# Performance work log

Hardware: AMD Instinct MI355X
Metric: run time of the kernel (lower is better)

The kernel has to match this reference:

```python
import jax, jax.numpy as jnp
import numpy as np

# Degree-sorted atom layout (DeepChem convention): atoms of degree d are contiguous.
D_COUNTS = [8192, 65536, 131072, 196608, 98304, 16384, 8192]  # degrees 0..6
OFFSETS = np.cumsum([0] + D_COUNTS)  # start index of each degree block
N_ATOMS = int(OFFSETS[-1])           # 524288
F_IN = 75
BATCH = 16384
MAX_DEG = 6
BN_EPS = 1e-3


def setup_inputs() -> dict:
    key = jax.random.key(0)
    ks = jax.random.split(key, 40)
    inp = {}
    inp["atom_features"] = jax.random.normal(ks[0], (N_ATOMS, F_IN), jnp.float32)
    # every molecule gets exactly N_ATOMS/BATCH atoms -> all segments populated
    inp["membership"] = (jnp.arange(N_ATOMS, dtype=jnp.int32) % BATCH)
    for d in range(1, MAX_DEG + 1):
        inp[f"adj{d}"] = jax.random.randint(ks[d], (D_COUNTS[d], d), 0, N_ATOMS, dtype=jnp.int32)
    # GraphConv weights: 2*MAX_DEG + 1 = 13 matrices (rel/self per degree 1..6, self for degree 0)
    inp["gc1_W"] = jax.random.normal(ks[10], (13, F_IN, 32), jnp.float32) * 0.1
    inp["gc1_b"] = jax.random.normal(ks[11], (13, 32), jnp.float32) * 0.01
    inp["gc2_W"] = jax.random.normal(ks[12], (13, 32, 32), jnp.float32) * 0.1
    inp["gc2_b"] = jax.random.normal(ks[13], (13, 32), jnp.float32) * 0.01
    inp["bn1_gamma"] = jnp.ones((32,), jnp.float32)
    inp["bn1_beta"] = jnp.zeros((32,), jnp.float32)
    inp["bn1_mean"] = jax.random.normal(ks[14], (32,), jnp.float32) * 0.1
    inp["bn1_var"] = jax.random.uniform(ks[15], (32,), jnp.float32, 0.5, 1.5)
    inp["bn3_gamma"] = jnp.ones((64,), jnp.float32)
    inp["bn3_beta"] = jnp.zeros((64,), jnp.float32)
    inp["bn3_mean"] = jax.random.normal(ks[16], (64,), jnp.float32) * 0.1
    inp["bn3_var"] = jax.random.uniform(ks[17], (64,), jnp.float32, 0.5, 1.5)
    inp["d1_W"] = jax.random.normal(ks[18], (32, 64), jnp.float32) * 0.1
    inp["d1_b"] = jnp.zeros((64,), jnp.float32)
    inp["d2_W"] = jax.random.normal(ks[19], (128, 1), jnp.float32) * 0.1
    inp["d2_b"] = jnp.zeros((1,), jnp.float32)
    inp["d3_W"] = jnp.array([0.5, -1, -1, 1, 1, 1, 1, 1, -1, -1, -1, -1, -1, -1, -1, -1], jnp.float32)[:, None]
    inp["d3_b"] = jnp.zeros((1,), jnp.float32)
    inp["x_add"] = jax.random.normal(ks[20], (BATCH, 15), jnp.float32)
    inp["batch_size"] = BATCH
    return inp


def _batch_norm(x, gamma, beta, mean, var):
    return gamma * (x - mean) * jax.lax.rsqrt(var + BN_EPS) + beta


def _graph_conv(atoms, adjs, W, b):
    # atoms: [N, F]; adjs[d-1]: [n_d, d] neighbor indices for degree-d atoms
    outs = []
    for d in range(1, MAX_DEG + 1):
        s, n = int(OFFSETS[d]), D_COUNTS[d]
        rel = atoms[adjs[d - 1]].sum(axis=1)          # [n_d, F] summed neighbors
        self_a = atoms[s:s + n]                        # [n_d, F]
        wr, br = W[2 * (d - 1)], b[2 * (d - 1)]
        ws, bs = W[2 * (d - 1) + 1], b[2 * (d - 1) + 1]
        outs.append(rel @ wr + br + self_a @ ws + bs)
    out0 = atoms[:D_COUNTS[0]] @ W[12] + b[12]         # degree-0: self only
    return jnp.tanh(jnp.concatenate([out0] + outs, axis=0))


def _graph_pool(atoms, adjs):
    outs = [atoms[:D_COUNTS[0]]]  # degree-0 passthrough
    for d in range(1, MAX_DEG + 1):
        s, n = int(OFFSETS[d]), D_COUNTS[d]
        self_a = atoms[s:s + n]
        neigh_max = atoms[adjs[d - 1]].max(axis=1)     # [n_d, F]
        outs.append(jnp.maximum(self_a, neigh_max))    # max over {self} U neighbors
    return jnp.concatenate(outs, axis=0)


def reference(atom_features, membership, adj1, adj2, adj3, adj4, adj5, adj6,
              gc1_W, gc1_b, gc2_W, gc2_b,
              bn1_gamma, bn1_beta, bn1_mean, bn1_var,
              bn3_gamma, bn3_beta, bn3_mean, bn3_var,
              d1_W, d1_b, d2_W, d2_b, d3_W, d3_b, x_add, batch_size):
    adjs = [adj1, adj2, adj3, adj4, adj5, adj6]
    h = _graph_conv(atom_features, adjs, gc1_W, gc1_b)          # [N, 32], tanh
    h = _batch_norm(h, bn1_gamma, bn1_beta, bn1_mean, bn1_var)
    h = _graph_pool(h, adjs)
    h = _graph_conv(h, adjs, gc2_W, gc2_b)                      # [N, 32]
    # NOTE: original reuses batch_norm1 here (source does self.batch_norm1 twice)
    h = _batch_norm(h, bn1_gamma, bn1_beta, bn1_mean, bn1_var)
    h = _graph_pool(h, adjs)
    h = jnp.tanh(h @ d1_W + d1_b)                               # [N, 64]
    h = _batch_norm(h, bn3_gamma, bn3_beta, bn3_mean, bn3_var)
    # GraphGather: per-molecule sum and max readout
    sum_r = jax.ops.segment_sum(h, membership, num_segments=batch_size)
    max_r = jax.ops.segment_max(h, membership, num_segments=batch_size)
    mol = jnp.tanh(jnp.concatenate([sum_r, max_r], axis=1))     # [B, 128]
    model_var = mol @ d2_W + d2_b                               # [B, 1]
    binding = jnp.concatenate([model_var, x_add], axis=1)       # [B, 16]
    ans = binding @ d3_W + d3_b                                 # [B, 1]
    return ans.reshape(1, -1)
```

## Files before the change

### kernel.cpp

```cpp
#include <hip/hip_runtime.h>

typedef unsigned short u16;
typedef __bf16 bf8v __attribute__((ext_vector_type(8)));
typedef float f32x4 __attribute__((ext_vector_type(4)));

#define N_ATOMS 524288
#define NROW32  16777216

#define P_EP1   0
#define P_EP2   224
#define P_BN1   448
#define P_BN3   576
#define P_D1WT  832
#define P_D1B   2880
#define P_D2W   2944
#define P_SC    3072

__device__ __forceinline__ float b2f(u16 u) {
  return __builtin_bit_cast(float, ((unsigned)u) << 16);
}
__device__ __forceinline__ u16 f2b(float f) {
  unsigned x = __builtin_bit_cast(unsigned, f);
  x += 0x7fffu + ((x >> 16) & 1u);
  return (u16)(x >> 16);
}
__device__ __forceinline__ float ldf(const void* p, size_t i, int isbf) {
  return isbf ? b2f(((const u16*)p)[i]) : ((const float*)p)[i];
}
__device__ __forceinline__ u16 ldb(const void* p, size_t i, int isbf) {
  return isbf ? ((const u16*)p)[i] : f2b(((const float*)p)[i]);
}

__device__ __forceinline__ float exp2_fast(float x) {
#if __has_builtin(__builtin_amdgcn_exp2f)
  return __builtin_amdgcn_exp2f(x);
#else
  return exp2f(x);
#endif
}
__device__ __forceinline__ float rcp_fast(float x) {
#if __has_builtin(__builtin_amdgcn_rcpf)
  return __builtin_amdgcn_rcpf(x);
#else
  return 1.0f / x;
#endif
}
__device__ __forceinline__ float tanh_fast(float x) {
  float xc = fminf(fmaxf(x, -15.f), 15.f);
  float t = exp2_fast(xc * -2.8853900817779268f);
  return (1.f - t) * rcp_fast(1.f + t);
}

__device__ __forceinline__ void seg_of(int r, int& d, int& off) {
  if      (r < 8192)   { d = 0; off = 0; }
  else if (r < 73728)  { d = 1; off = 8192; }
  else if (r < 204800) { d = 2; off = 73728; }
  else if (r < 401408) { d = 3; off = 204800; }
  else if (r < 499712) { d = 4; off = 401408; }
  else if (r < 516096) { d = 5; off = 499712; }
  else                 { d = 6; off = 516096; }
}

__global__ void probe_kernel(const void* __restrict__ atoms, int* __restrict__ flag) {
  int lane = threadIdx.x;
  unsigned u = ((const u16*)atoms)[(size_t)lane * 148];
  int e = (u >> 7) & 0xFF;
  bool ok = (e >= 100 && e <= 140);
  unsigned long long b = __ballot(ok);
  if (lane == 0) flag[0] = (__popcll(b) >= 48) ? 1 : 0;
}

__global__ __launch_bounds__(64) void prep_kernel(
    const void* gW1, const void* gB1, const void* gW2, const void* gB2,
    const void* b1g, const void* b1b, const void* b1m, const void* b1v,
    const void* g3, const void* b3, const void* m3, const void* v3,
    const void* d1W, const void* d1b, const void* d2W, const void* d2b,
    const void* d3W, const void* d3b,
    const int* flagp, char* ws)
{
  const int isbf = flagp[0];
  const int lane = threadIdx.x;
  float* P  = (float*)(ws + 256);
  u16* wf1 = (u16*)(ws + 16384);
  u16* wf2 = (u16*)(ws + 88064);
  const int blk = blockIdx.x;

  if (blk < 7) {
    const int d = blk;
    const int wr  = (d == 0) ? 12 : 2 * (d - 1);
    const int wsi = (d == 0) ? 12 : 2 * (d - 1) + 1;
    const int nl = lane & 15, q = lane >> 4;
    #pragma unroll
    for (int ks = 0; ks < 5; ++ks)
      #pragma unroll
      for (int ct = 0; ct < 2; ++ct) {
        u16* dst = wf1 + (size_t)(((d * 5 + ks) * 2 + ct) * 64 + lane) * 8;
        #pragma unroll
        for (int j = 0; j < 8; ++j) {
          int k = ks * 32 + q * 8 + j, n = ct * 16 + nl;
          u16 val = 0;
          if (k < 75) val = ldb(gW1, (size_t)wr * 2400 + k * 32 + n, isbf);
          else if (k >= 80 && k < 155) val = ldb(gW1, (size_t)wsi * 2400 + (k - 80) * 32 + n, isbf);
          dst[j] = val;
        }
      }
    #pragma unroll
    for (int ks = 0; ks < 2; ++ks)
      #pragma unroll
      for (int ct = 0; ct < 2; ++ct) {
        u16* dst = wf2 + (size_t)(((d * 2 + ks) * 2 + ct) * 64 + lane) * 8;
        #pragma unroll
        for (int j = 0; j < 8; ++j) {
          int k = ks * 32 + q * 8 + j, n = ct * 16 + nl;
          dst[j] = (k < 32) ? ldb(gW2, (size_t)wr * 1024 + k * 32 + n, isbf)
                            : ldb(gW2, (size_t)wsi * 1024 + (k - 32) * 32 + n, isbf);
        }
      }
    if (lane < 32) {
      int col = lane;
      float bb1 = (d == 0) ? ldf(gB1, 12 * 32 + col, isbf)
                           : ldf(gB1, wr * 32 + col, isbf) + ldf(gB1, wsi * 32 + col, isbf);
      float bb2 = (d == 0) ? ldf(gB2, 12 * 32 + col, isbf)
                           : ldf(gB2, wr * 32 + col, isbf) + ldf(gB2, wsi * 32 + col, isbf);
      P[P_EP1 + d * 32 + col] = bb1;
      P[P_EP2 + d * 32 + col] = bb2;
    }
  } else {
    if (lane < 32) {
      P[P_BN1 + lane]      = ldf(b1g, lane, isbf);
      P[P_BN1 + 32 + lane] = ldf(b1b, lane, isbf);
      P[P_BN1 + 64 + lane] = ldf(b1m, lane, isbf);
      P[P_BN1 + 96 + lane] = 1.0f / sqrtf(ldf(b1v, lane, isbf) + 0.001f);
    }
    P[P_BN3 + lane]       = ldf(g3, lane, isbf);
    P[P_BN3 + 64 + lane]  = ldf(b3, lane, isbf);
    P[P_BN3 + 128 + lane] = ldf(m3, lane, isbf);
    P[P_BN3 + 192 + lane] = 1.0f / sqrtf(ldf(v3, lane, isbf) + 0.001f);
    for (int k = 0; k < 32; ++k)
      P[P_D1WT + lane * 32 + k] = ldf(d1W, k * 64 + lane, isbf);
    P[P_D1B + lane] = ldf(d1b, lane, isbf);
    P[P_D2W + lane]      = ldf(d2W, lane, isbf);
    P[P_D2W + 64 + lane] = ldf(d2W, 64 + lane, isbf);
    if (lane < 16) P[P_SC + 1 + lane] = ldf(d3W, lane, isbf);
    if (lane == 0) { P[P_SC] = ldf(d2b, 0, isbf); P[P_SC + 17] = ldf(d3b, 0, isbf); }
  }
}

__global__ __launch_bounds__(256) void convert_kernel(
    const void* __restrict__ atoms, const int* flagp, u16* __restrict__ outB)
{
  __shared__ __align__(16) u16 sT[128 * 80];
  const int isbf = flagp[0];
  const int tid = threadIdx.x;
  const int rb = blockIdx.x * 128;

  for (int i = tid; i < 128 * 5; i += 256) {
    int rl = i / 5, k = 75 + (i % 5);
    sT[rl * 80 + k] = 0;
  }
  if (isbf) {
    const uint4* in4 = (const uint4*)((const u16*)atoms + (size_t)rb * 75);
    for (int i = tid; i < 1200; i += 256) {
      union { uint4 u4; u16 us[8]; } w; w.u4 = in4[i];
      int e0 = i * 8;
      #pragma unroll
      for (int j = 0; j < 8; ++j) {
        int e = e0 + j, rl = e / 75, k = e - rl * 75;
        sT[rl * 80 + k] = w.us[j];
      }
    }
  } else {
    const f32x4* in4 = (const f32x4*)((const float*)atoms + (size_t)rb * 75);
    for (int i = tid; i < 2400; i += 256) {
      f32x4 v = in4[i];
      int e0 = i * 4;
      #pragma unroll
      for (int j = 0; j < 4; ++j) {
        int e = e0 + j, rl = e / 75, k = e - rl * 75;
        sT[rl * 80 + k] = f2b(v[j]);
      }
    }
  }
  __syncthreads();
  uint4* dst = (uint4*)(outB + (size_t)rb * 80);
  const uint4* src = (const uint4*)sT;
  for (int i = tid; i < 1280; i += 256) dst[i] = src[i];
}

template<int D>
__device__ __forceinline__ void gather2_conv1(
    const u16* __restrict__ atomsB, const int* __restrict__ adjp,
    int r0, int r1, int off, int q, bf8v a0[5], bf8v a1[5])
{
  constexpr int DD = (D > 0) ? D : 1;
  int nb0[DD], nb1[DD];
  if (D > 0) {
    size_t i0 = (size_t)(r0 - off) * D, i1 = (size_t)(r1 - off) * D;
    #pragma unroll
    for (int j = 0; j < D; ++j) { nb0[j] = adjp[i0 + j]; nb1[j] = adjp[i1 + j]; }
  }
  const u16* s0 = atomsB + (size_t)r0 * 80;
  const u16* s1 = atomsB + (size_t)r1 * 80;
  #pragma unroll
  for (int ks = 0; ks < 5; ++ks) {
    const int c = ks * 32 + q * 8;
    if (c >= 80) {
      a0[ks] = *(const bf8v*)(s0 + (c - 80));
      a1[ks] = *(const bf8v*)(s1 + (c - 80));
    } else {
      uint4 v0[DD], v1[DD];
      #pragma unroll
      for (int j = 0; j < D; ++j) {
        v0[j] = *(const uint4*)(atomsB + (size_t)nb0[j] * 80 + c);
        v1[j] = *(const uint4*)(atomsB + (size_t)nb1[j] * 80 + c);
      }
      float r0s[8], r1s[8];
      #pragma unroll
      for (int i = 0; i < 8; ++i) { r0s[i] = 0.f; r1s[i] = 0.f; }
      #pragma unroll
      for (int j = 0; j < D; ++j) {
        union { uint4 u4; u16 us[8]; } a, b;
        a.u4 = v0[j]; b.u4 = v1[j];
        #pragma unroll
        for (int i = 0; i < 8; ++i) { r0s[i] += b2f(a.us[i]); r1s[i] += b2f(b.us[i]); }
      }
      union { u16 us[8]; bf8v v; } o0, o1;
      #pragma unroll
      for (int i = 0; i < 8; ++i) { o0.us[i] = f2b(r0s[i]); o1.us[i] = f2b(r1s[i]); }
      a0[ks] = o0.v; a1[ks] = o1.v;
    }
  }
}

__global__ __launch_bounds__(256) void conv1_fast_kernel(
    const u16* __restrict__ atomsB, const u16* __restrict__ wf1, const float* __restrict__ P,
    const int* __restrict__ a1p, const int* __restrict__ a2p, const int* __restrict__ a3p,
    const int* __restrict__ a4p, const int* __restrict__ a5p, const int* __restrict__ a6p,
    u16* __restrict__ out)
{
  const int tid = threadIdx.x;
  const int rb = blockIdx.x * 128;
  int d, off; seg_of(rb, d, off);
  const int lane = tid & 63;
  const int nl = lane & 15;
  const int q  = lane >> 4;
  const int wvid = tid >> 6;

  bf8v bfrag[5][2];
  #pragma unroll
  for (int ks = 0; ks < 5; ++ks)
    #pragma unroll
    for (int ct = 0; ct < 2; ++ct)
      bfrag[ks][ct] = *(const bf8v*)(wf1 + (size_t)(((d * 5 + ks) * 2 + ct) * 64 + lane) * 8);

  const int r0 = rb + wvid * 32 + nl;
  const int r1 = r0 + 16;
  bf8v a0[5], a1f[5];
  switch (d) {
    case 0: gather2_conv1<0>(atomsB, a1p, r0, r1, off, q, a0, a1f); break;
    case 1: gather2_conv1<1>(atomsB, a1p, r0, r1, off, q, a0, a1f); break;
    case 2: gather2_conv1<2>(atomsB, a2p, r0, r1, off, q, a0, a1f); break;
    case 3: gather2_conv1<3>(atomsB, a3p, r0, r1, off, q, a0, a1f); break;
    case 4: gather2_conv1<4>(atomsB, a4p, r0, r1, off, q, a0, a1f); break;
    case 5: gather2_conv1<5>(atomsB, a5p, r0, r1, off, q, a0, a1f); break;
    default: gather2_conv1<6>(atomsB, a6p, r0, r1, off, q, a0, a1f); break;
  }

  f32x4 acc[2][2] = {{{0,0,0,0},{0,0,0,0}},{{0,0,0,0},{0,0,0,0}}};
  #pragma unroll
  for (int ks = 0; ks < 5; ++ks) {
    acc[0][0] = __builtin_amdgcn_mfma_f32_16x16x32_bf16(a0[ks],  bfrag[ks][0], acc[0][0], 0, 0, 0);
    acc[0][1] = __builtin_amdgcn_mfma_f32_16x16x32_bf16(a0[ks],  bfrag[ks][1], acc[0][1], 0, 0, 0);
    acc[1][0] = __builtin_amdgcn_mfma_f32_16x16x32_bf16(a1f[ks], bfrag[ks][0], acc[1][0], 0, 0, 0);
    acc[1][1] = __builtin_amdgcn_mfma_f32_16x16x32_bf16(a1f[ks], bfrag[ks][1], acc[1][1], 0, 0, 0);
  }

  #pragma unroll
  for (int ct = 0; ct < 2; ++ct) {
    const int col = ct * 16 + nl;
    const float bias = P[P_EP1 + d * 32 + col];
    const float g  = P[P_BN1 + col];
    const float be = P[P_BN1 + 32 + col];
    const float mn = P[P_BN1 + 64 + col];
    const float iv = P[P_BN1 + 96 + col];
    #pragma unroll
    for (int t = 0; t < 2; ++t) {
      #pragma unroll
      for (int reg = 0; reg < 4; ++reg) {
        int row = rb + wvid * 32 + t * 16 + q * 4 + reg;
        float v = tanh_fast(acc[t][ct][reg] + bias);
        out[(size_t)row * 32 + col] = f2b(g * (v - mn) * iv + be);
      }
    }
  }
}

__global__ __launch_bounds__(256) void conv1_slow_kernel(
    const void* __restrict__ atoms, const void* __restrict__ gW, const void* __restrict__ gB,
    const void* __restrict__ bng, const void* __restrict__ bnb,
    const void* __restrict__ bnm, const void* __restrict__ bnv,
    const int* __restrict__ a1, const int* __restrict__ a2, const int* __restrict__ a3,
    const int* __restrict__ a4, const int* __restrict__ a5, const int* __restrict__ a6,
    const int* flagp, u16* __restrict__ out)
{
  __shared__ __align__(16) u16 sX[64 * 168];
  const int isbf = flagp[0];
  const int tid = threadIdx.x;
  const int rb = blockIdx.x * 64;
  int d, off; seg_of(rb, d, off);
  const int wr  = (d == 0) ? 12 : 2 * (d - 1);
  const int wsi = (d == 0) ? 12 : 2 * (d - 1) + 1;
  const size_t wrb = (size_t)wr  * 2400;
  const size_t wsb = (size_t)wsi * 2400;
  const int lane = tid & 63;
  const int nl = lane & 15;
  const int q  = lane >> 4;

  bf8v bfrag[5][2];
  #pragma unroll
  for (int ks = 0; ks < 5; ++ks)
    #pragma unroll
    for (int ct = 0; ct < 2; ++ct) {
      union { u16 u[8]; bf8v v; } tmp;
      #pragma unroll
      for (int j = 0; j < 8; ++j) {
        int k = ks * 32 + q * 8 + j, n = ct * 16 + nl;
        u16 val = 0;
        if (k < 75) val = ldb(gW, wrb + (size_t)k * 32 + n, isbf);
        else if (k >= 80 && k < 155) val = ldb(gW, wsb + (size_t)(k - 80) * 32 + n, isbf);
        tmp.u[j] = val;
      }
      bfrag[ks][ct] = tmp.v;
    }

  {
    const int lr = tid >> 2;
    const int kq = tid & 3;
    const int r  = rb + lr;
    int nb[6];
    if (d > 0) {
      const int* adjp = (d==1)?a1:(d==2)?a2:(d==3)?a3:(d==4)?a4:(d==5)?a5:a6;
      size_t ib = (size_t)(r - off) * d;
      for (int j = 0; j < d; ++j) nb[j] = adjp[ib + j];
    }
    u16* px = sX + lr * 168;
    for (int k = kq; k < 80; k += 4) {
      u16 sv = 0; float rs = 0.f;
      if (k < 75) {
        sv = ldb(atoms, (size_t)r * 75 + k, isbf);
        for (int j = 0; j < d; ++j) rs += ldf(atoms, (size_t)nb[j] * 75 + k, isbf);
      }
      px[80 + k] = sv;
      px[k]      = f2b(rs);
    }
  }
  __syncthreads();

  const int wvid = tid >> 6;
  f32x4 acc0 = {0.f, 0.f, 0.f, 0.f};
  f32x4 acc1 = {0.f, 0.f, 0.f, 0.f};
  const u16* abase = sX + (wvid * 16 + nl) * 168 + q * 8;
  #pragma unroll
  for (int ks = 0; ks < 5; ++ks) {
    bf8v a = *(const bf8v*)(abase + ks * 32);
    acc0 = __builtin_amdgcn_mfma_f32_16x16x32_bf16(a, bfrag[ks][0], acc0, 0, 0, 0);
    acc1 = __builtin_amdgcn_mfma_f32_16x16x32_bf16(a, bfrag[ks][1], acc1, 0, 0, 0);
  }
  #pragma unroll
  for (int ct = 0; ct < 2; ++ct) {
    f32x4 acc = ct ? acc1 : acc0;
    int col = ct * 16 + nl;
    float bias = (d == 0) ? ldf(gB, 12 * 32 + col, isbf)
                          : ldf(gB, wr * 32 + col, isbf) + ldf(gB, wsi * 32 + col, isbf);
    float g  = ldf(bng, col, isbf);
    float be = ldf(bnb, col, isbf);
    float mn = ldf(bnm, col, isbf);
    float iv = 1.0f / sqrtf(ldf(bnv, col, isbf) + 0.001f);
    #pragma unroll
    for (int reg = 0; reg < 4; ++reg) {
      int row = rb + wvid * 16 + q * 4 + reg;
      float t = tanh_fast(acc[reg] + bias);
      out[(size_t)row * 32 + col] = f2b(g * (t - mn) * iv + be);
    }
  }
}

template<int D>
__device__ __forceinline__ void gather2_conv2(
    const u16* __restrict__ in, const int* __restrict__ adjp,
    int r0, int r1, int off, int q, bf8v a0[2], bf8v a1[2])
{
  constexpr int DD = (D > 0) ? D : 1;
  int nb0[DD], nb1[DD];
  if (D > 0) {
    size_t i0 = (size_t)(r0 - off) * D, i1 = (size_t)(r1 - off) * D;
    #pragma unroll
    for (int j = 0; j < D; ++j) { nb0[j] = adjp[i0 + j]; nb1[j] = adjp[i1 + j]; }
  }
  a0[1] = *(const bf8v*)(in + (size_t)r0 * 32 + q * 8);
  a1[1] = *(const bf8v*)(in + (size_t)r1 * 32 + q * 8);
  uint4 v0[DD], v1[DD];
  #pragma unroll
  for (int j = 0; j < D; ++j) {
    v0[j] = *(const uint4*)(in + (size_t)nb0[j] * 32 + q * 8);
    v1[j] = *(const uint4*)(in + (size_t)nb1[j] * 32 + q * 8);
  }
  float r0s[8], r1s[8];
  #pragma unroll
  for (int i = 0; i < 8; ++i) { r0s[i] = 0.f; r1s[i] = 0.f; }
  #pragma unroll
  for (int j = 0; j < D; ++j) {
    union { uint4 u4; u16 us[8]; } a, b;
    a.u4 = v0[j]; b.u4 = v1[j];
    #pragma unroll
    for (int i = 0; i < 8; ++i) { r0s[i] += b2f(a.us[i]); r1s[i] += b2f(b.us[i]); }
  }
  union { u16 us[8]; bf8v v; } o0, o1;
  #pragma unroll
  for (int i = 0; i < 8; ++i) { o0.us[i] = f2b(r0s[i]); o1.us[i] = f2b(r1s[i]); }
  a0[0] = o0.v; a1[0] = o1.v;
}

__global__ __launch_bounds__(256) void conv2_kernel(
    const u16* __restrict__ in, const u16* __restrict__ wf2, const float* __restrict__ P,
    const int* __restrict__ a1p, const int* __restrict__ a2p, const int* __restrict__ a3p,
    const int* __restrict__ a4p, const int* __restrict__ a5p, const int* __restrict__ a6p,
    u16* __restrict__ out)
{
  const int tid = threadIdx.x;
  const int rb = blockIdx.x * 128;
  int d, off; seg_of(rb, d, off);
  const int lane = tid & 63;
  const int nl = lane & 15;
  const int q  = lane >> 4;
  const int wvid = tid >> 6;

  bf8v bfrag[2][2];
  #pragma unroll
  for (int ks = 0; ks < 2; ++ks)
    #pragma unroll
    for (int ct = 0; ct < 2; ++ct)
      bfrag[ks][ct] = *(const bf8v*)(wf2 + (size_t)(((d * 2 + ks) * 2 + ct) * 64 + lane) * 8);

  const int r0 = rb + wvid * 32 + nl;
  const int r1 = r0 + 16;
  bf8v a0[2], a1f[2];
  switch (d) {
    case 0: gather2_conv2<0>(in, a1p, r0, r1, off, q, a0, a1f); break;
    case 1: gather2_conv2<1>(in, a1p, r0, r1, off, q, a0, a1f); break;
    case 2: gather2_conv2<2>(in, a2p, r0, r1, off, q, a0, a1f); break;
    case 3: gather2_conv2<3>(in, a3p, r0, r1, off, q, a0, a1f); break;
    case 4: gather2_conv2<4>(in, a4p, r0, r1, off, q, a0, a1f); break;
    case 5: gather2_conv2<5>(in, a5p, r0, r1, off, q, a0, a1f); break;
    default: gather2_conv2<6>(in, a6p, r0, r1, off, q, a0, a1f); break;
  }

  f32x4 acc[2][2] = {{{0,0,0,0},{0,0,0,0}},{{0,0,0,0},{0,0,0,0}}};
  #pragma unroll
  for (int ks = 0; ks < 2; ++ks) {
    acc[0][0] = __builtin_amdgcn_mfma_f32_16x16x32_bf16(a0[ks],  bfrag[ks][0], acc[0][0], 0, 0, 0);
    acc[0][1] = __builtin_amdgcn_mfma_f32_16x16x32_bf16(a0[ks],  bfrag[ks][1], acc[0][1], 0, 0, 0);
    acc[1][0] = __builtin_amdgcn_mfma_f32_16x16x32_bf16(a1f[ks], bfrag[ks][0], acc[1][0], 0, 0, 0);
    acc[1][1] = __builtin_amdgcn_mfma_f32_16x16x32_bf16(a1f[ks], bfrag[ks][1], acc[1][1], 0, 0, 0);
  }

  #pragma unroll
  for (int ct = 0; ct < 2; ++ct) {
    const int col = ct * 16 + nl;
    const float bias = P[P_EP2 + d * 32 + col];
    const float g  = P[P_BN1 + col];
    const float be = P[P_BN1 + 32 + col];
    const float mn = P[P_BN1 + 64 + col];
    const float iv = P[P_BN1 + 96 + col];
    #pragma unroll
    for (int t = 0; t < 2; ++t) {
      #pragma unroll
      for (int reg = 0; reg < 4; ++reg) {
        int row = rb + wvid * 32 + t * 16 + q * 4 + reg;
        float v = tanh_fast(acc[t][ct][reg] + bias);
        out[(size_t)row * 32 + col] = f2b(g * (v - mn) * iv + be);
      }
    }
  }
}

template<int D>
__device__ __forceinline__ void pool_one(
    const u16* __restrict__ in, const int* __restrict__ adjp,
    int r, int off, int q8, u16* __restrict__ out)
{
  constexpr int DD = (D > 0) ? D : 1;
  int nb[DD];
  if (D > 0) {
    size_t ib = (size_t)(r - off) * D;
    #pragma unroll
    for (int j = 0; j < D; ++j) nb[j] = adjp[ib + j];
  }
  uint4 sv = *(const uint4*)(in + (size_t)r * 32 + q8);
  uint4 nv[DD];
  #pragma unroll
  for (int j = 0; j < D; ++j) nv[j] = *(const uint4*)(in + (size_t)nb[j] * 32 + q8);
  union { uint4 u4; u16 us[8]; } s; s.u4 = sv;
  float v[8];
  #pragma unroll
  for (int i = 0; i < 8; ++i) v[i] = b2f(s.us[i]);
  #pragma unroll
  for (int j = 0; j < D; ++j) {
    union { uint4 u4; u16 us[8]; } a; a.u4 = nv[j];
    #pragma unroll
    for (int i = 0; i < 8; ++i) v[i] = fmaxf(v[i], b2f(a.us[i]));
  }
  union { uint4 u4; u16 us[8]; } o;
  #pragma unroll
  for (int i = 0; i < 8; ++i) o.us[i] = f2b(v[i]);
  *(uint4*)(out + (size_t)r * 32 + q8) = o.u4;
}

__global__ __launch_bounds__(256) void pool_kernel(
    const u16* __restrict__ in, u16* __restrict__ out,
    const int* __restrict__ a1, const int* __restrict__ a2, const int* __restrict__ a3,
    const int* __restrict__ a4, const int* __restrict__ a5, const int* __restrict__ a6)
{
  int idx = blockIdx.x * 256 + threadIdx.x;
  int r = idx >> 2, q8 = (idx & 3) * 8;
  int d, off; seg_of(r, d, off);
  switch (d) {
    case 0: pool_one<0>(in, a1, r, off, q8, out); break;
    case 1: pool_one<1>(in, a1, r, off, q8, out); break;
    case 2: pool_one<2>(in, a2, r, off, q8, out); break;
    case 3: pool_one<3>(in, a3, r, off, q8, out); break;
    case 4: pool_one<4>(in, a4, r, off, q8, out); break;
    case 5: pool_one<5>(in, a5, r, off, q8, out); break;
    default: pool_one<6>(in, a6, r, off, q8, out); break;
  }
}

__global__ __launch_bounds__(256) void head_kernel(
    const u16* __restrict__ in, const float* __restrict__ P,
    const void* __restrict__ xadd, const int* flagp, void* __restrict__ outp)
{
  __shared__ __align__(16) float sA[4][1024];
  const int isbf = flagp[0];
  const int wvid = threadIdx.x >> 6;
  const int m = blockIdx.x * 4 + wvid;
  const int j = threadIdx.x & 63;

  #pragma unroll
  for (int ii = 0; ii < 2; ++ii) {
    int i = j + ii * 64;
    int t = i >> 2, kq8 = (i & 3) * 8;
    union { uint4 u4; u16 us[8]; } w;
    w.u4 = *(const uint4*)(in + (size_t)(m + t * 16384) * 32 + kq8);
    #pragma unroll
    for (int x = 0; x < 8; ++x) sA[wvid][t * 32 + kq8 + x] = b2f(w.us[x]);
  }
  __syncthreads();

  float wcol[32];
  const f32x4* wt4 = (const f32x4*)(P + P_D1WT + j * 32);
  #pragma unroll
  for (int k4 = 0; k4 < 8; ++k4) {
    f32x4 w4 = wt4[k4];
    wcol[k4 * 4] = w4[0]; wcol[k4 * 4 + 1] = w4[1];
    wcol[k4 * 4 + 2] = w4[2]; wcol[k4 * 4 + 3] = w4[3];
  }
  const float bj = P[P_D1B + j];
  const float g  = P[P_BN3 + j];
  const float bt = P[P_BN3 + 64 + j];
  const float mn = P[P_BN3 + 128 + j];
  const float iv = P[P_BN3 + 192 + j];

  float sum = 0.f, mx = -1e30f;
  for (int t = 0; t < 32; ++t) {
    const f32x4* arow = (const f32x4*)(&sA[wvid][t * 32]);
    float dot = bj;
    #pragma unroll
    for (int k4 = 0; k4 < 8; ++k4) {
      f32x4 av = arow[k4];
      dot += av[0] * wcol[k4 * 4]     + av[1] * wcol[k4 * 4 + 1]
           + av[2] * wcol[k4 * 4 + 2] + av[3] * wcol[k4 * 4 + 3];
    }
    float h  = tanh_fast(dot);
    float hb = g * (h - mn) * iv + bt;
    sum += hb;
    mx = fmaxf(mx, hb);
  }

  float part = tanh_fast(sum) * P[P_D2W + j] + tanh_fast(mx) * P[P_D2W + 64 + j];
  #pragma unroll
  for (int o = 32; o > 0; o >>= 1) part += __shfl_down(part, o, 64);

  if (j == 0) {
    float mv  = part + P[P_SC];
    float ans = mv * P[P_SC + 1] + P[P_SC + 17];
    #pragma unroll
    for (int i = 0; i < 15; ++i) ans += ldf(xadd, m * 15 + i, isbf) * P[P_SC + 2 + i];
    if (isbf) ((u16*)outp)[m] = f2b(ans);
    else      ((float*)outp)[m] = ans;
  }
}

extern "C" void kernel_launch(void* const* d_in, const int* in_sizes, int n_in,
                              void* d_out, int out_size, void* d_ws, size_t ws_size,
                              hipStream_t stream)
{
  (void)in_sizes; (void)n_in; (void)out_size;
  const void* atoms = d_in[0];
  const int* a1 = (const int*)d_in[2];
  const int* a2 = (const int*)d_in[3];
  const int* a3 = (const int*)d_in[4];
  const int* a4 = (const int*)d_in[5];
  const int* a5 = (const int*)d_in[6];
  const int* a6 = (const int*)d_in[7];

  char* ws = (char*)d_ws;
  int*  flag = (int*)ws;
  float* P   = (float*)(ws + 256);
  u16*  wf1  = (u16*)(ws + 16384);
  u16*  wf2  = (u16*)(ws + 88064);
  u16*  buf0 = (u16*)(ws + 131072);

  const size_t need = 131072 + (size_t)NROW32 * 2 + (size_t)N_ATOMS * 80 * 2;
  const bool fast = ws_size >= need;

  probe_kernel<<<1, 64, 0, stream>>>(atoms, flag);
  prep_kernel<<<8, 64, 0, stream>>>(d_in[8], d_in[9], d_in[10], d_in[11],
                                    d_in[12], d_in[13], d_in[14], d_in[15],
                                    d_in[16], d_in[17], d_in[18], d_in[19],
                                    d_in[20], d_in[21], d_in[22], d_in[23],
                                    d_in[24], d_in[25], flag, ws);

  u16* buf1;
  if (fast) {
    u16* atomsB = buf0 + NROW32;
    buf1 = atomsB;
    convert_kernel<<<4096, 256, 0, stream>>>(atoms, flag, atomsB);
    conv1_fast_kernel<<<4096, 256, 0, stream>>>(atomsB, wf1, P,
                                                a1, a2, a3, a4, a5, a6, buf0);
  } else {
    buf1 = buf0 + NROW32;
    conv1_slow_kernel<<<8192, 256, 0, stream>>>(atoms, d_in[8], d_in[9], d_in[12],
                                                d_in[13], d_in[14], d_in[15],
                                                a1, a2, a3, a4, a5, a6, flag, buf0);
  }

  pool_kernel<<<8192, 256, 0, stream>>>(buf0, buf1, a1, a2, a3, a4, a5, a6);
  conv2_kernel<<<4096, 256, 0, stream>>>(buf1, wf2, P, a1, a2, a3, a4, a5, a6, buf0);
  pool_kernel<<<8192, 256, 0, stream>>>(buf0, buf1, a1, a2, a3, a4, a5, a6);
  head_kernel<<<4096, 256, 0, stream>>>(buf1, P, d_in[26], flag, d_out);
}
```

Baseline: 558.5 us.

## Fuse second graph pool into head kernel and use native bf16 conversion

Removes the second pool_kernel launch and folds its neighbor-max gather into the head kernel's load stage, so pooled features are computed on the fly from the conv2 output. This avoids writing and re-reading a full N×32 bf16 intermediate buffer. The head kernel now does per-atom degree lookup and divergent gathers inside each wave, which may reduce coalescing. The float-to-bf16 rounding helper is also replaced with the compiler's native conversion.

Result: faster. 540.9 us (-3.1%).

```diff
diff --git a/kernel.cpp b/kernel.cpp
--- a/kernel.cpp
+++ b/kernel.cpp
@@ -20,9 +20,7 @@
   return __builtin_bit_cast(float, ((unsigned)u) << 16);
 }
 __device__ __forceinline__ u16 f2b(float f) {
-  unsigned x = __builtin_bit_cast(unsigned, f);
-  x += 0x7fffu + ((x >> 16) & 1u);
-  return (u16)(x >> 16);
+  return __builtin_bit_cast(u16, (__bf16)f);
 }
 __device__ __forceinline__ float ldf(const void* p, size_t i, int isbf) {
   return isbf ? b2f(((const u16*)p)[i]) : ((const float*)p)[i];
@@ -537,6 +535,8 @@
 
 __global__ __launch_bounds__(256) void head_kernel(
     const u16* __restrict__ in, const float* __restrict__ P,
+    const int* __restrict__ a1, const int* __restrict__ a2, const int* __restrict__ a3,
+    const int* __restrict__ a4, const int* __restrict__ a5, const int* __restrict__ a6,
     const void* __restrict__ xadd, const int* flagp, void* __restrict__ outp)
 {
   __shared__ __align__(16) float sA[4][1024];
@@ -549,10 +549,26 @@
   for (int ii = 0; ii < 2; ++ii) {
     int i = j + ii * 64;
     int t = i >> 2, kq8 = (i & 3) * 8;
+    int r = m + t * 16384;
+    int d, off; seg_of(r, d, off);
     union { uint4 u4; u16 us[8]; } w;
-    w.u4 = *(const uint4*)(in + (size_t)(m + t * 16384) * 32 + kq8);
-    #pragma unroll
-    for (int x = 0; x < 8; ++x) sA[wvid][t * 32 + kq8 + x] = b2f(w.us[x]);
+    w.u4 = *(const uint4*)(in + (size_t)r * 32 + kq8);
+    float v[8];
+    #pragma unroll
+    for (int x = 0; x < 8; ++x) v[x] = b2f(w.us[x]);
+    if (d > 0) {
+      const int* adjp = (d==1)?a1:(d==2)?a2:(d==3)?a3:(d==4)?a4:(d==5)?a5:a6;
+      size_t ib = (size_t)(r - off) * d;
+      for (int jn = 0; jn < d; ++jn) {
+        int nb = adjp[ib + jn];
+        union { uint4 u4; u16 us[8]; } a;
+        a.u4 = *(const uint4*)(in + (size_t)nb * 32 + kq8);
+        #pragma unroll
+        for (int x = 0; x < 8; ++x) v[x] = fmaxf(v[x], b2f(a.us[x]));
+      }
+    }
+    #pragma unroll
+    for (int x = 0; x < 8; ++x) sA[wvid][t * 32 + kq8 + x] = v[x];
   }
   __syncthreads();
 
@@ -646,6 +662,6 @@
 
   pool_kernel<<<8192, 256, 0, stream>>>(buf0, buf1, a1, a2, a3, a4, a5, a6);
   conv2_kernel<<<4096, 256, 0, stream>>>(buf1, wf2, P, a1, a2, a3, a4, a5, a6, buf0);
-  pool_kernel<<<8192, 256, 0, stream>>>(buf0, buf1, a1, a2, a3, a4, a5, a6);
-  head_kernel<<<4096, 256, 0, stream>>>(buf1, P, d_in[26], flag, d_out);
-}
+  head_kernel<<<4096, 256, 0, stream>>>(buf0, P, a1, a2, a3, a4, a5, a6,
+                                        d_in[26], flag, d_out);
+}
```
